# Performance work log

Measured on AMD Instinct MI355X. Metric: run time of the kernel, lower is better.

## Reference

```python
import jax, jax.numpy as jnp
import numpy as np

B, S, D = 4, 2048, 1024
H, HD = 16, 64  # num_head, head_dim


def setup_inputs() -> dict:
    key = jax.random.key(0)
    ks = jax.random.split(key, 6)
    scale = 1.0 / np.sqrt(D)
    X = jax.random.normal(ks[0], (B, S, D), dtype=jnp.float32)
    mask = jnp.ones((B, S), dtype=jnp.float32)
    Wq = jax.random.normal(ks[1], (D, H * HD), dtype=jnp.float32) * scale
    Wk = jax.random.normal(ks[2], (D, H * HD), dtype=jnp.float32) * scale
    Wv = jax.random.normal(ks[3], (D, H * HD), dtype=jnp.float32) * scale
    Wo = jax.random.normal(ks[4], (H * HD, D), dtype=jnp.float32) * scale
    bq = jnp.zeros((H * HD,), jnp.float32)
    bk = jnp.zeros((H * HD,), jnp.float32)
    bv = jnp.zeros((H * HD,), jnp.float32)
    bo = jnp.zeros((D,), jnp.float32)
    return {"X": X, "mask": mask, "Wq": Wq, "bq": bq, "Wk": Wk, "bk": bk,
            "Wv": Wv, "bv": bv, "Wo": Wo, "bo": bo}


def _split_heads(t):
    # [B, S, H*HD] -> [B, H, S, HD]
    return t.reshape(B, S, H, HD).transpose(0, 2, 1, 3)


def reference(X, mask, Wq, bq, Wk, bk, Wv, bv, Wo, bo):
    Q = _split_heads(X @ Wq + bq)
    K = _split_heads(X @ Wk + bk)
    V = _split_heads(X @ Wv + bv)
    # scaled dot-product with additive mask penalty (faithful to source)
    dot = jnp.einsum('bhqd,bhkd->bhqk', Q, K) / np.sqrt(HD)
    dot = dot - 1e6 * (1.0 - mask[:, None, None, :])
    attn = jax.nn.softmax(dot, axis=-1)
    ctx = jnp.einsum('bhqk,bhkd->bhqd', attn, V)
    # combine heads: [B,H,S,HD] -> [B,S,H*HD]
    ctx = ctx.transpose(0, 2, 1, 3).reshape(B, S, H * HD)
    return ctx @ Wo + bo
```

## Files before the change

kernel.cpp:

```cpp
#include <hip/hip_runtime.h>
#include <hip/hip_bf16.h>
#include <stdint.h>

typedef __bf16 bf16x8 __attribute__((ext_vector_type(8)));
typedef short  s16x8  __attribute__((ext_vector_type(8)));
typedef float  f32x4  __attribute__((ext_vector_type(4)));
typedef float  f32x16 __attribute__((ext_vector_type(16)));
typedef unsigned int u32x2 __attribute__((ext_vector_type(2)));
typedef unsigned int u32x4 __attribute__((ext_vector_type(4)));

__device__ __forceinline__ f32x4 mfma16(s16x8 a, s16x8 b, f32x4 c) {
  return __builtin_amdgcn_mfma_f32_16x16x32_bf16(
      __builtin_bit_cast(bf16x8, a), __builtin_bit_cast(bf16x8, b), c, 0, 0, 0);
}
__device__ __forceinline__ f32x16 mfma32(s16x8 a, s16x8 b, f32x16 c) {
  return __builtin_amdgcn_mfma_f32_32x32x16_bf16(
      __builtin_bit_cast(bf16x8, a), __builtin_bit_cast(bf16x8, b), c, 0, 0, 0);
}

__device__ __forceinline__ void load_lds16(const void* g, void* l) {
  __builtin_amdgcn_global_load_lds(
      (const __attribute__((address_space(1))) void*)g,
      (__attribute__((address_space(3))) void*)l,
      16, 0, 0);
}

__device__ __forceinline__ float exp2fast(float x) {
  float r; asm("v_exp_f32 %0, %1" : "=v"(r) : "v"(x)); return r;
}
__device__ __forceinline__ unsigned cvtpk_bf16(float lo, float hi) {
  unsigned r; asm("v_cvt_pk_bf16_f32 %0, %1, %2" : "=v"(r) : "v"(lo), "v"(hi)); return r;
}
__device__ __forceinline__ void plswap2(unsigned a, unsigned b, int hi,
                                        unsigned& x, unsigned& y) {
#if __has_builtin(__builtin_amdgcn_permlane32_swap)
  auto r = __builtin_amdgcn_permlane32_swap(a, b, false, false);
  x = (unsigned)r[0]; y = (unsigned)r[1];
#else
  unsigned ax = (unsigned)__shfl_xor((int)a, 32);
  unsigned bx = (unsigned)__shfl_xor((int)b, 32);
  x = hi ? bx : a;
  y = hi ? b : ax;
#endif
}

__global__ void cvt_x(const float* __restrict__ in, __hip_bfloat16* __restrict__ out, int n) {
  int i = (blockIdx.x * 256 + threadIdx.x) << 2;
  if (i >= n) return;
  float4 v = *(const float4*)(in + i);
  out[i + 0] = __float2bfloat16(v.x);
  out[i + 1] = __float2bfloat16(v.y);
  out[i + 2] = __float2bfloat16(v.z);
  out[i + 3] = __float2bfloat16(v.w);
}

__global__ void cvt_w_t(const float* __restrict__ in, __hip_bfloat16* __restrict__ out) {
  __shared__ float t[64][65];
  const int tx = threadIdx.x & 63, ty = threadIdx.x >> 6;
  const int bk = blockIdx.x & 15, bn = blockIdx.x >> 4;
  const int k0 = bk * 64, n0 = bn * 64;
#pragma unroll
  for (int j = 0; j < 16; ++j)
    t[ty + j * 4][tx] = in[(size_t)(k0 + ty + j * 4) * 1024 + n0 + tx];
  __syncthreads();
#pragma unroll
  for (int j = 0; j < 16; ++j)
    out[(size_t)(n0 + ty + j * 4) * 1024 + k0 + tx] =
        __float2bfloat16(t[tx][ty + j * 4]);
}

template <int OUT_MODE>
__launch_bounds__(256, 2)
__global__ void gemm_bt(const __hip_bfloat16* __restrict__ A,
                        const __hip_bfloat16* __restrict__ Bt,
                        const float* __restrict__ bias,
                        void* __restrict__ Cout,
                        int M, int N, int K) {
  __shared__ __align__(16) __hip_bfloat16 As[128 * 64];
  __shared__ __align__(16) __hip_bfloat16 Bs[128 * 64];
  const int tid  = threadIdx.x;
  const int lane = tid & 63;
  const int wv   = tid >> 6;
  const int l15  = lane & 15;
  const int lhi  = lane >> 4;

  const int tilesN = N >> 7;
  const int bm = blockIdx.x / tilesN;
  const int bn = blockIdx.x % tilesN;
  const int m0 = bm << 7, n0 = bn << 7;
  const int wr = wv >> 1, wc = wv & 1;

  f32x4 acc[4][4];
  const f32x4 z = {0.f, 0.f, 0.f, 0.f};
#pragma unroll
  for (int i = 0; i < 4; ++i)
#pragma unroll
    for (int j = 0; j < 4; ++j) acc[i][j] = z;

  const int lrow = lane >> 3;
  const int seg2 = (lane & 7) ^ lrow;
  const int nkt = K >> 6;

  for (int kt = 0; kt < nkt; ++kt) {
    __syncthreads();
    const int gk = (kt << 6) + (seg2 << 3);
#pragma unroll
    for (int j = 0; j < 4; ++j) {
      const int c = (wv << 2) + j;
      const int row = (c << 3) + lrow;
      load_lds16(A  + (size_t)(m0 + row) * K + gk, &As[c << 9]);
      load_lds16(Bt + (size_t)(n0 + row) * K + gk, &Bs[c << 9]);
    }
    __syncthreads();

#pragma unroll
    for (int kk = 0; kk < 2; ++kk) {
      s16x8 af[4], bfr[4];
#pragma unroll
      for (int mi = 0; mi < 4; ++mi) {
        const int row = (wr << 6) + (mi << 4) + l15;
        const int off = (row << 7) + ((((kk << 2) | lhi) ^ (row & 7)) << 4);
        af[mi] = *(const s16x8*)((const char*)As + off);
      }
#pragma unroll
      for (int ni = 0; ni < 4; ++ni) {
        const int row = (wc << 6) + (ni << 4) + l15;
        const int off = (row << 7) + ((((kk << 2) | lhi) ^ (row & 7)) << 4);
        bfr[ni] = *(const s16x8*)((const char*)Bs + off);
      }
#pragma unroll
      for (int mi = 0; mi < 4; ++mi)
#pragma unroll
        for (int ni = 0; ni < 4; ++ni)
          acc[mi][ni] = mfma16(af[mi], bfr[ni], acc[mi][ni]);
    }
  }

#pragma unroll
  for (int ni = 0; ni < 4; ++ni) {
    const int col = n0 + (wc << 6) + (ni << 4) + l15;
    const float bval = bias ? bias[col] : 0.f;
    if (OUT_MODE == 1) {
      const int h = col >> 6, d = col & 63;
#pragma unroll
      for (int mi = 0; mi < 4; ++mi) {
        const int row0 = m0 + (wr << 6) + (mi << 4) + (lhi << 2);
#pragma unroll
        for (int r = 0; r < 4; ++r) {
          const int row = row0 + r;
          const int bb = row >> 11, s = row & 2047;
          ((__hip_bfloat16*)Cout)[(((size_t)(bb * 16 + h) * 64 + d) << 11) + s] =
              __float2bfloat16(acc[mi][ni][r] + bval);
        }
      }
    } else {
#pragma unroll
      for (int mi = 0; mi < 4; ++mi) {
        const int row0 = m0 + (wr << 6) + (mi << 4) + (lhi << 2);
#pragma unroll
        for (int r = 0; r < 4; ++r) {
          const float v = acc[mi][ni][r] + bval;
          if (OUT_MODE == 0)
            ((__hip_bfloat16*)Cout)[(size_t)(row0 + r) * N + col] = __float2bfloat16(v);
          else
            ((float*)Cout)[(size_t)(row0 + r) * N + col] = v;
        }
      }
    }
  }
}

__launch_bounds__(256, 2)
__global__ void attn32(const __hip_bfloat16* __restrict__ Qb,
                       const __hip_bfloat16* __restrict__ Kb,
                       const __hip_bfloat16* __restrict__ Vt,
                       const float* __restrict__ mask,
                       __hip_bfloat16* __restrict__ ctx) {
  __shared__ __align__(16) __hip_bfloat16 K_lds[2][4096];
  __shared__ __align__(16) __hip_bfloat16 V_lds[2][4096];
  __shared__ float pen_lds[2048];

  const int tid = threadIdx.x;
  const int lane = tid & 63, wv = tid >> 6;
  const int l31 = lane & 31, hi = lane >> 5;

  const int bid = blockIdx.x;
  const int lb = (bid & 7) * 128 + (bid >> 3);
  const int qt = lb & 15;
  const int bh = lb >> 4;
  const int h = bh & 15, b = bh >> 4;

  const int srow = lane >> 3;
  const int sseg = (lane & 7) ^ srow;
  const char* kg[2];
  const char* vg[2];
#pragma unroll
  for (int p = 0; p < 2; ++p) {
    const int row = (p * 4 + wv) * 8 + srow;
    kg[p] = (const char*)Kb +
            (((size_t)(b * 2048 + row) << 10) + h * 64 + sseg * 8) * 2;
    vg[p] = (const char*)Vt +
            (((size_t)(bh * 64 + row) << 11) + sseg * 8) * 2;
  }

  int offs[8];
#pragma unroll
  for (int i = 0; i < 8; ++i) {
    const int row7 = l31 & 7;
    offs[i] = ((i >> 2) << 12) + (l31 << 7) +
              ((((((i & 3) << 1) | hi)) ^ row7) << 4);
  }

#pragma unroll
  for (int p = 0; p < 2; ++p) {
    load_lds16(kg[p], &K_lds[0][(p * 4 + wv) * 512]);
    load_lds16(vg[p], &V_lds[0][(p * 4 + wv) * 512]);
  }
  {
    const float* mrow = mask + b * 2048;
    const int i0 = tid * 8;
    float4 m0 = *(const float4*)(mrow + i0);
    float4 m1 = *(const float4*)(mrow + i0 + 4);
    pen_lds[i0 + 0] = fmaf(m0.x, 1442695.04f, -1442711.04f);
    pen_lds[i0 + 1] = fmaf(m0.y, 1442695.04f, -1442711.04f);
    pen_lds[i0 + 2] = fmaf(m0.z, 1442695.04f, -1442711.04f);
    pen_lds[i0 + 3] = fmaf(m0.w, 1442695.04f, -1442711.04f);
    pen_lds[i0 + 4] = fmaf(m1.x, 1442695.04f, -1442711.04f);
    pen_lds[i0 + 5] = fmaf(m1.y, 1442695.04f, -1442711.04f);
    pen_lds[i0 + 6] = fmaf(m1.z, 1442695.04f, -1442711.04f);
    pen_lds[i0 + 7] = fmaf(m1.w, 1442695.04f, -1442711.04f);
  }

  const int q0 = qt * 128 + wv * 32;

  s16x8 qf[4];
  {
    const __hip_bfloat16* qp =
        Qb + (size_t)(b * 2048 + q0 + l31) * 1024 + h * 64 + hi * 8;
#pragma unroll
    for (int d = 0; d < 4; ++d) qf[d] = *(const s16x8*)(qp + d * 16);
  }

  f32x16 oa0, oa1;
#pragma unroll
  for (int i = 0; i < 16; ++i) { oa0[i] = 0.f; oa1[i] = 0.f; }
  float lsum[4] = {0.f, 0.f, 0.f, 0.f};

  __syncthreads();

  for (int t = 0; t < 32; ++t) {
    const int cur = t & 1;
    if (t < 31) {
      const size_t kadv = (size_t)(t + 1) << 17;
      const size_t vadv = (size_t)(t + 1) << 7;
#pragma unroll
      for (int p = 0; p < 2; ++p) {
        load_lds16(kg[p] + kadv, &K_lds[cur ^ 1][(p * 4 + wv) * 512]);
        load_lds16(vg[p] + vadv, &V_lds[cur ^ 1][(p * 4 + wv) * 512]);
      }
    }

    const char* kb = (const char*)K_lds[cur];
    f32x16 sa[2];
#pragma unroll
    for (int i = 0; i < 16; ++i) { sa[0][i] = 0.f; sa[1][i] = 0.f; }
    {
      s16x8 kf[4];
#pragma unroll
      for (int i = 0; i < 4; ++i) kf[i] = *(const s16x8*)(kb + offs[i]);
      __builtin_amdgcn_s_setprio(1);
#pragma unroll
      for (int d = 0; d < 4; ++d) sa[0] = mfma32(kf[d], qf[d], sa[0]);
      __builtin_amdgcn_s_setprio(0);
#pragma unroll
      for (int i = 0; i < 4; ++i) kf[i] = *(const s16x8*)(kb + offs[4 + i]);
      __builtin_amdgcn_s_setprio(1);
#pragma unroll
      for (int d = 0; d < 4; ++d) sa[1] = mfma32(kf[d], qf[d], sa[1]);
      __builtin_amdgcn_s_setprio(0);
    }

    const int k0 = t << 6;
    float pq[32];
#pragma unroll
    for (int s = 0; s < 2; ++s)
#pragma unroll
      for (int a = 0; a < 4; ++a) {
        const f32x4 pn = *(const f32x4*)&pen_lds[k0 + s * 32 + a * 8 + hi * 4];
#pragma unroll
        for (int r = 0; r < 4; ++r) {
          const float p =
              exp2fast(fmaf(sa[s][a * 4 + r], 0.18033688011112042f, pn[r]));
          pq[s * 16 + a * 4 + r] = p;
          lsum[r] += p;
        }
      }

    s16x8 pb[4];
#pragma unroll
    for (int ks = 0; ks < 4; ++ks) {
      const int base = (ks >> 1) * 16 + (ks & 1) * 8;
      const unsigned wa0 = cvtpk_bf16(pq[base + 0], pq[base + 1]);
      const unsigned wa1 = cvtpk_bf16(pq[base + 2], pq[base + 3]);
      const unsigned wb0 = cvtpk_bf16(pq[base + 4], pq[base + 5]);
      const unsigned wb1 = cvtpk_bf16(pq[base + 6], pq[base + 7]);
      unsigned x0, y0, x1, y1;
      plswap2(wa0, wb0, hi, x0, y0);
      plswap2(wa1, wb1, hi, x1, y1);
      u32x4 u = {x0, x1, y0, y1};
      pb[ks] = __builtin_bit_cast(s16x8, u);
    }

    const char* vb = (const char*)V_lds[cur];
    {
      s16x8 vf[4];
#pragma unroll
      for (int i = 0; i < 4; ++i) vf[i] = *(const s16x8*)(vb + offs[i]);
      __builtin_amdgcn_s_setprio(1);
#pragma unroll
      for (int ks = 0; ks < 4; ++ks) oa0 = mfma32(vf[ks], pb[ks], oa0);
      __builtin_amdgcn_s_setprio(0);
#pragma unroll
      for (int i = 0; i < 4; ++i) vf[i] = *(const s16x8*)(vb + offs[4 + i]);
      __builtin_amdgcn_s_setprio(1);
#pragma unroll
      for (int ks = 0; ks < 4; ++ks) oa1 = mfma32(vf[ks], pb[ks], oa1);
      __builtin_amdgcn_s_setprio(0);
    }

    __syncthreads();
  }

  float lrun = (lsum[0] + lsum[1]) + (lsum[2] + lsum[3]);
  lrun += __shfl_xor(lrun, 32);
  const float inv = 1.0f / lrun;
  __hip_bfloat16* cp = ctx + (size_t)(b * 2048 + q0 + l31) * 1024 + h * 64 + hi * 4;
#pragma unroll
  for (int dt = 0; dt < 2; ++dt) {
#pragma unroll
    for (int g = 0; g < 4; ++g) {
      const float v0 = (dt ? oa1[4 * g + 0] : oa0[4 * g + 0]) * inv;
      const float v1 = (dt ? oa1[4 * g + 1] : oa0[4 * g + 1]) * inv;
      const float v2 = (dt ? oa1[4 * g + 2] : oa0[4 * g + 2]) * inv;
      const float v3 = (dt ? oa1[4 * g + 3] : oa0[4 * g + 3]) * inv;
      u32x2 u;
      u[0] = cvtpk_bf16(v0, v1);
      u[1] = cvtpk_bf16(v2, v3);
      *(u32x2*)(cp + dt * 32 + g * 8) = u;
    }
  }
}

extern "C" void kernel_launch(void* const* d_in, const int* in_sizes, int n_in,
                              void* d_out, int out_size, void* d_ws, size_t ws_size,
                              hipStream_t stream) {
  const float* X    = (const float*)d_in[0];
  const float* mask = (const float*)d_in[1];
  const float* Wq   = (const float*)d_in[2];
  const float* bq   = (const float*)d_in[3];
  const float* Wk   = (const float*)d_in[4];
  const float* bk   = (const float*)d_in[5];
  const float* Wv   = (const float*)d_in[6];
  const float* bvv  = (const float*)d_in[7];
  const float* Wo   = (const float*)d_in[8];
  const float* bo   = (const float*)d_in[9];
  float* out = (float*)d_out;
  char* ws = (char*)d_ws;

  __hip_bfloat16* Xb  = (__hip_bfloat16*)(ws + 0);
  __hip_bfloat16* ctx = Xb;
  __hip_bfloat16* Wqt = (__hip_bfloat16*)(ws + 16777216);
  __hip_bfloat16* Wkt = (__hip_bfloat16*)(ws + 18874368);
  __hip_bfloat16* Wvt = (__hip_bfloat16*)(ws + 20971520);
  __hip_bfloat16* Wot = (__hip_bfloat16*)(ws + 23068672);
  __hip_bfloat16* Qb  = (__hip_bfloat16*)(ws + 25165824);
  __hip_bfloat16* Kb  = (__hip_bfloat16*)(ws + 41943040);
  __hip_bfloat16* Vt  = (__hip_bfloat16*)(ws + 58720256);

  cvt_x<<<8192, 256, 0, stream>>>(X, Xb, 8388608);
  cvt_w_t<<<256, 256, 0, stream>>>(Wq, Wqt);
  cvt_w_t<<<256, 256, 0, stream>>>(Wk, Wkt);
  cvt_w_t<<<256, 256, 0, stream>>>(Wv, Wvt);
  cvt_w_t<<<256, 256, 0, stream>>>(Wo, Wot);

  gemm_bt<0><<<512, 256, 0, stream>>>(Xb, Wqt, bq,  Qb,  8192, 1024, 1024);
  gemm_bt<0><<<512, 256, 0, stream>>>(Xb, Wkt, bk,  Kb,  8192, 1024, 1024);
  gemm_bt<1><<<512, 256, 0, stream>>>(Xb, Wvt, bvv, Vt,  8192, 1024, 1024);

  attn32<<<1024, 256, 0, stream>>>(Qb, Kb, Vt, mask, ctx);

  gemm_bt<2><<<512, 256, 0, stream>>>(ctx, Wot, bo, out, 8192, 1024, 1024);
}
```

Baseline: 212.6 us.

## Fuse QKV projections into one GEMM launch and batch weight conversions

Merges the four weight transpose/convert launches into a single kernel over a concatenated weight buffer, and replaces the three separate Q/K/V GEMM launches with one gemm_qkv launch over N=3072 that selects bias and output layout per column block. Both GEMMs also get an XCD-aware block index remap so that neighbouring tiles land on the same chiplet for L2 reuse, plus compile-time constant strides. This cuts launch count and tail effects, and lets the shared X tile be reused across the Q, K and V columns. The cost is some per-block branching in the epilogue.

```diff
diff --git a/kernel.cpp b/kernel.cpp
--- a/kernel.cpp
+++ b/kernel.cpp
@@ -54,10 +54,16 @@
   out[i + 3] = __float2bfloat16(v.w);
 }
 
-__global__ void cvt_w_t(const float* __restrict__ in, __hip_bfloat16* __restrict__ out) {
+__global__ void cvt_w_t4(const float* __restrict__ W0, const float* __restrict__ W1,
+                         const float* __restrict__ W2, const float* __restrict__ W3,
+                         __hip_bfloat16* __restrict__ outbase) {
   __shared__ float t[64][65];
+  const int sel = blockIdx.x >> 8;
+  const int bid = blockIdx.x & 255;
+  const float* in = sel == 0 ? W0 : sel == 1 ? W1 : sel == 2 ? W2 : W3;
+  __hip_bfloat16* out = outbase + (size_t)sel * 1048576;
   const int tx = threadIdx.x & 63, ty = threadIdx.x >> 6;
-  const int bk = blockIdx.x & 15, bn = blockIdx.x >> 4;
+  const int bk = bid & 15, bn = bid >> 4;
   const int k0 = bk * 64, n0 = bn * 64;
 #pragma unroll
   for (int j = 0; j < 16; ++j)
@@ -69,13 +75,15 @@
         __float2bfloat16(t[tx][ty + j * 4]);
 }
 
-template <int OUT_MODE>
 __launch_bounds__(256, 2)
-__global__ void gemm_bt(const __hip_bfloat16* __restrict__ A,
-                        const __hip_bfloat16* __restrict__ Bt,
-                        const float* __restrict__ bias,
-                        void* __restrict__ Cout,
-                        int M, int N, int K) {
+__global__ void gemm_qkv(const __hip_bfloat16* __restrict__ A,
+                         const __hip_bfloat16* __restrict__ Bt,
+                         const float* __restrict__ bq,
+                         const float* __restrict__ bk,
+                         const float* __restrict__ bv,
+                         __hip_bfloat16* __restrict__ Qb,
+                         __hip_bfloat16* __restrict__ Kb,
+                         __hip_bfloat16* __restrict__ Vt) {
   __shared__ __align__(16) __hip_bfloat16 As[128 * 64];
   __shared__ __align__(16) __hip_bfloat16 Bs[128 * 64];
   const int tid  = threadIdx.x;
@@ -84,9 +92,10 @@
   const int l15  = lane & 15;
   const int lhi  = lane >> 4;
 
-  const int tilesN = N >> 7;
-  const int bm = blockIdx.x / tilesN;
-  const int bn = blockIdx.x % tilesN;
+  const int bid = blockIdx.x;
+  const int lb = (bid & 7) * 192 + (bid >> 3);
+  const int bm = lb / 24;
+  const int bn = lb % 24;
   const int m0 = bm << 7, n0 = bn << 7;
   const int wr = wv >> 1, wc = wv & 1;
 
@@ -99,17 +108,16 @@
 
   const int lrow = lane >> 3;
   const int seg2 = (lane & 7) ^ lrow;
-  const int nkt = K >> 6;
-
-  for (int kt = 0; kt < nkt; ++kt) {
+
+  for (int kt = 0; kt < 16; ++kt) {
     __syncthreads();
     const int gk = (kt << 6) + (seg2 << 3);
 #pragma unroll
     for (int j = 0; j < 4; ++j) {
       const int c = (wv << 2) + j;
       const int row = (c << 3) + lrow;
-      load_lds16(A  + (size_t)(m0 + row) * K + gk, &As[c << 9]);
-      load_lds16(Bt + (size_t)(n0 + row) * K + gk, &Bs[c << 9]);
+      load_lds16(A  + (((size_t)(m0 + row)) << 10) + gk, &As[c << 9]);
+      load_lds16(Bt + (((size_t)(n0 + row)) << 10) + gk, &Bs[c << 9]);
     }
     __syncthreads();
 
@@ -136,12 +144,15 @@
     }
   }
 
+  const int sel = n0 >> 10;
+  const float* bp = sel == 0 ? bq : sel == 1 ? bk : bv;
 #pragma unroll
   for (int ni = 0; ni < 4; ++ni) {
     const int col = n0 + (wc << 6) + (ni << 4) + l15;
-    const float bval = bias ? bias[col] : 0.f;
-    if (OUT_MODE == 1) {
-      const int h = col >> 6, d = col & 63;
+    const int c10 = col & 1023;
+    const float bval = bp[c10];
+    if (sel == 2) {
+      const int h = c10 >> 6, d = c10 & 63;
 #pragma unroll
       for (int mi = 0; mi < 4; ++mi) {
         const int row0 = m0 + (wr << 6) + (mi << 4) + (lhi << 2);
@@ -149,23 +160,99 @@
         for (int r = 0; r < 4; ++r) {
           const int row = row0 + r;
           const int bb = row >> 11, s = row & 2047;
-          ((__hip_bfloat16*)Cout)[(((size_t)(bb * 16 + h) * 64 + d) << 11) + s] =
+          Vt[(((size_t)(bb * 16 + h) * 64 + d) << 11) + s] =
               __float2bfloat16(acc[mi][ni][r] + bval);
         }
       }
     } else {
+      __hip_bfloat16* dst = sel == 0 ? Qb : Kb;
 #pragma unroll
       for (int mi = 0; mi < 4; ++mi) {
         const int row0 = m0 + (wr << 6) + (mi << 4) + (lhi << 2);
 #pragma unroll
-        for (int r = 0; r < 4; ++r) {
-          const float v = acc[mi][ni][r] + bval;
-          if (OUT_MODE == 0)
-            ((__hip_bfloat16*)Cout)[(size_t)(row0 + r) * N + col] = __float2bfloat16(v);
-          else
-            ((float*)Cout)[(size_t)(row0 + r) * N + col] = v;
-        }
-      }
+        for (int r = 0; r < 4; ++r)
+          dst[(((size_t)(row0 + r)) << 10) + c10] =
+              __float2bfloat16(acc[mi][ni][r] + bval);
+      }
+    }
+  }
+}
+
+__launch_bounds__(256, 2)
+__global__ void gemm_out(const __hip_bfloat16* __restrict__ A,
+                         const __hip_bfloat16* __restrict__ Bt,
+                         const float* __restrict__ bias,
+                         float* __restrict__ Cout) {
+  __shared__ __align__(16) __hip_bfloat16 As[128 * 64];
+  __shared__ __align__(16) __hip_bfloat16 Bs[128 * 64];
+  const int tid  = threadIdx.x;
+  const int lane = tid & 63;
+  const int wv   = tid >> 6;
+  const int l15  = lane & 15;
+  const int lhi  = lane >> 4;
+
+  const int bid = blockIdx.x;
+  const int lb = (bid & 7) * 64 + (bid >> 3);
+  const int bm = lb >> 3;
+  const int bn = lb & 7;
+  const int m0 = bm << 7, n0 = bn << 7;
+  const int wr = wv >> 1, wc = wv & 1;
+
+  f32x4 acc[4][4];
+  const f32x4 z = {0.f, 0.f, 0.f, 0.f};
+#pragma unroll
+  for (int i = 0; i < 4; ++i)
+#pragma unroll
+    for (int j = 0; j < 4; ++j) acc[i][j] = z;
+
+  const int lrow = lane >> 3;
+  const int seg2 = (lane & 7) ^ lrow;
+
+  for (int kt = 0; kt < 16; ++kt) {
+    __syncthreads();
+    const int gk = (kt << 6) + (seg2 << 3);
+#pragma unroll
+    for (int j = 0; j < 4; ++j) {
+      const int c = (wv << 2) + j;
+      const int row = (c << 3) + lrow;
+      load_lds16(A  + (((size_t)(m0 + row)) << 10) + gk, &As[c << 9]);
+      load_lds16(Bt + (((size_t)(n0 + row)) << 10) + gk, &Bs[c << 9]);
+    }
+    __syncthreads();
+
+#pragma unroll
+    for (int kk = 0; kk < 2; ++kk) {
+      s16x8 af[4], bfr[4];
+#pragma unroll
+      for (int mi = 0; mi < 4; ++mi) {
+        const int row = (wr << 6) + (mi << 4) + l15;
+        const int off = (row << 7) + ((((kk << 2) | lhi) ^ (row & 7)) << 4);
+        af[mi] = *(const s16x8*)((const char*)As + off);
+      }
+#pragma unroll
+      for (int ni = 0; ni < 4; ++ni) {
+        const int row = (wc << 6) + (ni << 4) + l15;
+        const int off = (row << 7) + ((((kk << 2) | lhi) ^ (row & 7)) << 4);
+        bfr[ni] = *(const s16x8*)((const char*)Bs + off);
+      }
+#pragma unroll
+      for (int mi = 0; mi < 4; ++mi)
+#pragma unroll
+        for (int ni = 0; ni < 4; ++ni)
+          acc[mi][ni] = mfma16(af[mi], bfr[ni], acc[mi][ni]);
+    }
+  }
+
+#pragma unroll
+  for (int ni = 0; ni < 4; ++ni) {
+    const int col = n0 + (wc << 6) + (ni << 4) + l15;
+    const float bval = bias[col];
+#pragma unroll
+    for (int mi = 0; mi < 4; ++mi) {
+      const int row0 = m0 + (wr << 6) + (mi << 4) + (lhi << 2);
+#pragma unroll
+      for (int r = 0; r < 4; ++r)
+        Cout[(((size_t)(row0 + r)) << 10) + col] = acc[mi][ni][r] + bval;
     }
   }
 }
@@ -367,27 +454,20 @@
   float* out = (float*)d_out;
   char* ws = (char*)d_ws;
 
-  __hip_bfloat16* Xb  = (__hip_bfloat16*)(ws + 0);
-  __hip_bfloat16* ctx = Xb;
-  __hip_bfloat16* Wqt = (__hip_bfloat16*)(ws + 16777216);
-  __hip_bfloat16* Wkt = (__hip_bfloat16*)(ws + 18874368);
-  __hip_bfloat16* Wvt = (__hip_bfloat16*)(ws + 20971520);
-  __hip_bfloat16* Wot = (__hip_bfloat16*)(ws + 23068672);
-  __hip_bfloat16* Qb  = (__hip_bfloat16*)(ws + 25165824);
-  __hip_bfloat16* Kb  = (__hip_bfloat16*)(ws + 41943040);
-  __hip_bfloat16* Vt  = (__hip_bfloat16*)(ws + 58720256);
+  __hip_bfloat16* Xb   = (__hip_bfloat16*)(ws + 0);
+  __hip_bfloat16* ctx  = Xb;
+  __hip_bfloat16* Wcat = (__hip_bfloat16*)(ws + 16777216);
+  __hip_bfloat16* Wot  = (__hip_bfloat16*)(ws + 23068672);
+  __hip_bfloat16* Qb   = (__hip_bfloat16*)(ws + 25165824);
+  __hip_bfloat16* Kb   = (__hip_bfloat16*)(ws + 41943040);
+  __hip_bfloat16* Vt   = (__hip_bfloat16*)(ws + 58720256);
 
   cvt_x<<<8192, 256, 0, stream>>>(X, Xb, 8388608);
-  cvt_w_t<<<256, 256, 0, stream>>>(Wq, Wqt);
-  cvt_w_t<<<256, 256, 0, stream>>>(Wk, Wkt);
-  cvt_w_t<<<256, 256, 0, stream>>>(Wv, Wvt);
-  cvt_w_t<<<256, 256, 0, stream>>>(Wo, Wot);
-
-  gemm_bt<0><<<512, 256, 0, stream>>>(Xb, Wqt, bq,  Qb,  8192, 1024, 1024);
-  gemm_bt<0><<<512, 256, 0, stream>>>(Xb, Wkt, bk,  Kb,  8192, 1024, 1024);
-  gemm_bt<1><<<512, 256, 0, stream>>>(Xb, Wvt, bvv, Vt,  8192, 1024, 1024);
+  cvt_w_t4<<<1024, 256, 0, stream>>>(Wq, Wk, Wv, Wo, Wcat);
+
+  gemm_qkv<<<1536, 256, 0, stream>>>(Xb, Wcat, bq, bk, bvv, Qb, Kb, Vt);
 
   attn32<<<1024, 256, 0, stream>>>(Qb, Kb, Vt, mask, ctx);
 
-  gemm_bt<2><<<512, 256, 0, stream>>>(ctx, Wot, bo, out, 8192, 1024, 1024);
-}
+  gemm_out<<<512, 256, 0, stream>>>(ctx, Wot, bo, out);
+}
```

New measurement: 187.9 us. -11.6%, faster.
